# Optimization experiments

Hardware: AMD Instinct MI355X
Metric: run time of the kernel (lower is better)

The kernel has to match this reference:

```python
import jax, jax.numpy as jnp
import numpy as np

N_NODES = 100000
N_EDGES = 1600000
N_PAIRS = 500000
K_HOPS = 6


def _bn(x, g, b, eps):
    # training-mode batch norm over the node/edge (batch) axis, biased variance
    mu = jnp.mean(x, axis=0)
    var = jnp.var(x, axis=0)
    return (x - mu) * jax.lax.rsqrt(var + eps) * g + b


def _gelu(x):
    return jax.nn.gelu(x, approximate=False)  # torch GELU default (erf)


def setup_inputs() -> dict:
    key = jax.random.key(0)
    ks = jax.random.split(key, 20)
    F, EF = 128, 32

    def w(k, shape, s=0.05):
        return jax.random.normal(k, shape, dtype=jnp.float32) * s

    return {
        'X': jax.random.normal(ks[0], (N_NODES, F), jnp.float32),
        'Y': jax.random.normal(ks[1], (N_PAIRS, EF), jnp.float32),
        'edge_index': jax.random.randint(ks[2], (2, N_EDGES), 0, N_NODES, jnp.int32),
        'inds0': jax.random.randint(ks[3], (N_PAIRS,), 0, N_NODES, jnp.int32),
        'inds1': jax.random.randint(ks[4], (N_PAIRS,), 0, N_NODES, jnp.int32),
        'bn_node_g': jnp.ones((F,), jnp.float32),
        'bn_node_b': jnp.zeros((F,), jnp.float32),
        'tag_lin_W': w(ks[5], (F, 128)),
        'tag_lin_b': jnp.zeros((128,), jnp.float32),
        'tag_Ws': w(ks[6], (K_HOPS + 1, 128, 128)),
        'tag_bias': jnp.zeros((128,), jnp.float32),
        'nl_W0': w(ks[7], (256, 256)),
        'nl_b0': jnp.zeros((256,), jnp.float32),
        'nl_W1': w(ks[8], (256, 128)),
        'nl_b1': jnp.zeros((128,), jnp.float32),
        'cl_W': w(ks[9], (128, 128)),
        'cl_b': jnp.zeros((128,), jnp.float32),
        'end_W': w(ks[10], (128, 8)),
        'end_b': jnp.zeros((8,), jnp.float32),
        'bn_edge_g': jnp.ones((544,), jnp.float32),
        'bn_edge_b': jnp.zeros((544,), jnp.float32),
        'el_W0': w(ks[11], (544, 512)),
        'el_b0': jnp.zeros((512,), jnp.float32),
        'el_W1': w(ks[12], (512, 256)),
        'el_b1': jnp.zeros((256,), jnp.float32),
        'el_end_W': w(ks[13], (256, 1)),
        'el_end_b': jnp.zeros((1,), jnp.float32),
    }


def reference(X, Y, bn_node_g, bn_node_b, tag_lin_W, tag_lin_b, tag_Ws, tag_bias,
              nl_W0, nl_b0, nl_W1, nl_b1, cl_W, cl_b, end_W, end_b,
              bn_edge_g, bn_edge_b, el_W0, el_b0, el_W1, el_b1, el_end_W, el_end_b,
              edge_index, inds0, inds1):
    N = X.shape[0]
    # ---- NodeGLAM ----
    x = _bn(X, bn_node_g, bn_node_b, 1e-5)
    # TagModule: Linear -> GELU -> TAGConv -> GELU
    h = _gelu(x @ tag_lin_W + tag_lin_b)
    src, dst = edge_index[0], edge_index[1]
    # gcn_norm (no self loops): deg over target, norm = d^-1/2[src]*d^-1/2[dst]
    deg = jax.ops.segment_sum(jnp.ones(src.shape, h.dtype), dst, num_segments=N)
    dinv = jnp.where(deg > 0, jax.lax.rsqrt(jnp.maximum(deg, 1.0)), 0.0)
    wgt = (dinv[src] * dinv[dst])[:, None]  # [E,1]
    out = h @ tag_Ws[0]
    hk = h
    for k in range(1, K_HOPS + 1):
        hk = jax.ops.segment_sum(hk[src] * wgt, dst, num_segments=N)  # gather-scale-scatter
        out = out + hk @ tag_Ws[k]
    h = _gelu(out + tag_bias)
    a = jnp.concatenate([x, h], axis=1)  # [N, 256]
    a = _gelu(a @ nl_W0 + nl_b0)
    a = _gelu(a @ nl_W1 + nl_b1)  # Node_embs [N,128]
    cl = _gelu(a @ cl_W + cl_b)
    node_classes = jax.nn.softmax(cl @ end_W + end_b, axis=-1)  # [N,8]
    # ---- edge feature gather + EdgeGLAM ----
    Omega = jnp.concatenate([a[inds0], a[inds1], X[inds0], X[inds1], Y], axis=1)  # [P,544]
    o = _bn(Omega, bn_edge_g, bn_edge_b, 1.0)  # BatchNorm(input_, output_) -> eps=1
    o = _gelu(o @ el_W0 + el_b0)
    o = _gelu(o @ el_W1 + el_b1)
    e_pred = jax.nn.sigmoid(o @ el_end_W + el_end_b)[:, 0]  # [P]
    return (node_classes, e_pred)
```

## Files before the change

### kernel.cpp

```cpp
#include <hip/hip_runtime.h>
#include <math.h>

#define NN 100000
#define NE 1600000
#define NP 500000
#define KHOPS 6
#define ECHK 50000
#define NB_SCAN ((NN + 1023) / 1024)

typedef unsigned short u16;
typedef short bf16x8 __attribute__((ext_vector_type(8)));
typedef float f32x4 __attribute__((ext_vector_type(4)));

__device__ __forceinline__ float gelu_erf(float x) {
    return 0.5f * x * (1.0f + erff(x * 0.70710678118654752f));
}
__device__ __forceinline__ float b2f(u16 u) {
    return __uint_as_float(((unsigned int)u) << 16);
}
__device__ __forceinline__ u16 f2b(float f) {
    unsigned int x = __float_as_uint(f);
    return (u16)((x + 0x7FFFu + ((x >> 16) & 1u)) >> 16);
}
__device__ __forceinline__ bf16x8 cvt8(float4 a, float4 b) {
    bf16x8 v;
    v[0]=(short)f2b(a.x); v[1]=(short)f2b(a.y); v[2]=(short)f2b(a.z); v[3]=(short)f2b(a.w);
    v[4]=(short)f2b(b.x); v[5]=(short)f2b(b.y); v[6]=(short)f2b(b.z); v[7]=(short)f2b(b.w);
    return v;
}

template<int BF>
__global__ void col_stats(const void* __restrict__ Matv, int rows, int lc,
                          const int* __restrict__ w0, const int* __restrict__ w1,
                          float* __restrict__ sums, float* __restrict__ sumsq,
                          int base0, int base1)
{
    __shared__ float red[256];
    const int t = threadIdx.x;
    const int C = 1 << lc;
    const long total = (long)rows << lc;
    const long stride = (long)gridDim.x * 256;
    float s0 = 0.f, q0 = 0.f, s1 = 0.f, q1 = 0.f;
    for (long idx = (long)blockIdx.x * 256 + t; idx < total; idx += stride) {
        int r = (int)(idx >> lc);
        float v = BF ? b2f(((const u16*)Matv)[idx]) : ((const float*)Matv)[idx];
        float f0 = w0 ? (float)w0[r] : 1.0f;
        s0 += f0 * v;
        q0 += f0 * v * v;
        if (w1) {
            float f1 = (float)w1[r];
            s1 += f1 * v;
            q1 += f1 * v * v;
        }
    }
    red[t] = s0; __syncthreads();
    if (t < C) { float x = 0.f; for (int k = t; k < 256; k += C) x += red[k]; atomicAdd(&sums[base0 + t], x); }
    __syncthreads();
    red[t] = q0; __syncthreads();
    if (t < C) { float x = 0.f; for (int k = t; k < 256; k += C) x += red[k]; atomicAdd(&sumsq[base0 + t], x); }
    __syncthreads();
    if (w1) {
        red[t] = s1; __syncthreads();
        if (t < C) { float x = 0.f; for (int k = t; k < 256; k += C) x += red[k]; atomicAdd(&sums[base1 + t], x); }
        __syncthreads();
        red[t] = q1; __syncthreads();
        if (t < C) { float x = 0.f; for (int k = t; k < 256; k += C) x += red[k]; atomicAdd(&sumsq[base1 + t], x); }
    }
}

__global__ void bn_finalize(const float* __restrict__ sums, const float* __restrict__ sumsq,
                            const float* __restrict__ g, const float* __restrict__ b,
                            float* __restrict__ s, float* __restrict__ t,
                            int C, float count, float eps)
{
    int c = blockIdx.x * blockDim.x + threadIdx.x;
    if (c < C) {
        float mu = sums[c] / count;
        float var = sumsq[c] / count - mu * mu;
        float sc = g[c] * rsqrtf(var + eps);
        s[c] = sc;
        t[c] = b[c] - mu * sc;
    }
}

__global__ void hist_add(const int* __restrict__ idx, int n, int* __restrict__ cnt)
{
    int stride = gridDim.x * blockDim.x;
    for (int i = blockIdx.x * blockDim.x + threadIdx.x; i < n; i += stride)
        atomicAdd(&cnt[idx[i]], 1);
}

__global__ void hist_add2(const int* __restrict__ i0, const int* __restrict__ i1, int n,
                          int* __restrict__ c0, int* __restrict__ c1)
{
    int stride = gridDim.x * blockDim.x;
    for (int i = blockIdx.x * blockDim.x + threadIdx.x; i < n; i += stride) {
        atomicAdd(&c0[i0[i]], 1);
        atomicAdd(&c1[i1[i]], 1);
    }
}

__global__ void scan1(const int* __restrict__ cnt, int* __restrict__ ex,
                      int* __restrict__ part, int n)
{
    __shared__ int buf[1024];
    int b = blockIdx.x, t = threadIdx.x;
    int i = b * 1024 + t;
    int v = (i < n) ? cnt[i] : 0;
    buf[t] = v;
    __syncthreads();
    int incl = v;
    for (int o = 1; o < 1024; o <<= 1) {
        int tmp = (t >= o) ? buf[t - o] : 0;
        __syncthreads();
        incl += tmp;
        buf[t] = incl;
        __syncthreads();
    }
    if (i < n) ex[i] = incl - v;
    if (t == 1023) part[b] = incl;
}

__global__ void scan2(int* __restrict__ part, int nb)
{
    __shared__ int s[256];
    int t = threadIdx.x;
    if (t < nb) s[t] = part[t];
    __syncthreads();
    if (t == 0) {
        int run = 0;
        for (int b = 0; b < nb; ++b) { int x = s[b]; part[b] = run; run += x; }
        part[nb] = run;
    }
}

__global__ void scan3(int* __restrict__ indptr, const int* __restrict__ part,
                      const int* __restrict__ cnt, float* __restrict__ dinv, int n)
{
    int b = blockIdx.x, t = threadIdx.x;
    int i = b * 1024 + t;
    if (i < n) {
        indptr[i] += part[b];
        int c = cnt[i];
        dinv[i] = (c > 0) ? rsqrtf((float)c) : 0.f;
    }
    if (b == 0 && t == 0) indptr[n] = part[NB_SCAN];
}

__global__ void csr_build(const int* __restrict__ src, const int* __restrict__ dst, int n,
                          const int* __restrict__ indptr, int* __restrict__ cursor,
                          int* __restrict__ csrS)
{
    int stride = gridDim.x * blockDim.x;
    for (int e = blockIdx.x * blockDim.x + threadIdx.x; e < n; e += stride) {
        int s = src[e], d = dst[e];
        int pos = indptr[d] + atomicAdd(&cursor[d], 1);
        csrS[pos] = s;
    }
}

__global__ void spmm_hop(const u16* __restrict__ hin, u16* __restrict__ hout,
                         const int* __restrict__ indptr, const int* __restrict__ csrS,
                         const float* __restrict__ dinv)
{
    int gid = blockIdx.x * blockDim.x + threadIdx.x;
    int node = gid >> 6;
    int lane = gid & 63;
    if (node >= NN) return;
    float dn = dinv[node];
    int beg = indptr[node], end = indptr[node + 1];
    float a0 = 0.f, a1 = 0.f;
    int e = beg;
    for (; e + 7 < end; e += 8) {
        int sidx[8];
        ushort2 pv[8];
#pragma unroll
        for (int u = 0; u < 8; ++u) sidx[u] = csrS[e + u];
#pragma unroll
        for (int u = 0; u < 8; ++u)
            pv[u] = *(const ushort2*)(hin + (size_t)sidx[u] * 128 + lane * 2);
#pragma unroll
        for (int u = 0; u < 8; ++u) {
            float wv = dn * dinv[sidx[u]];
            a0 = fmaf(wv, b2f(pv[u].x), a0);
            a1 = fmaf(wv, b2f(pv[u].y), a1);
        }
    }
    for (; e < end; ++e) {
        int s0 = csrS[e];
        float w0 = dn * dinv[s0];
        ushort2 p0 = *(const ushort2*)(hin + (size_t)s0 * 128 + lane * 2);
        a0 = fmaf(w0, b2f(p0.x), a0);
        a1 = fmaf(w0, b2f(p0.y), a1);
    }
    ushort2 o;
    o.x = f2b(a0); o.y = f2b(a1);
    *(ushort2*)(hout + (size_t)node * 128 + lane * 2) = o;
}

__global__ void convTB(const float* __restrict__ in, u16* __restrict__ out,
                       int K, int Nc, int B)
{
    int per = K * Nc;
    int i = blockIdx.x * blockDim.x + threadIdx.x;
    if (i < per * B) {
        int m = i / per, r = i - m * per;
        int n = r / K, k = r - n * K;
        out[i] = f2b(in[(size_t)m * per + (size_t)k * Nc + n]);
    }
}

__global__ void conv_pair(const float* __restrict__ Ws, u16* __restrict__ out)
{
    int i = blockIdx.x * blockDim.x + threadIdx.x;
    if (i < 3 * 128 * 256) {
        int p = i >> 15;
        int r = i & 32767;
        int n = r >> 8, k = r & 255;
        int hop = 2 * p + (k >> 7);
        out[i] = f2b(Ws[(size_t)hop * 16384 + (size_t)(k & 127) * 128 + n]);
    }
}

__global__ void convB(const float* __restrict__ in, u16* __restrict__ out, int n4)
{
    int stride = gridDim.x * blockDim.x;
    for (int i = blockIdx.x * blockDim.x + threadIdx.x; i < n4; i += stride) {
        float4 v = ((const float4*)in)[i];
        ushort4 o;
        o.x = f2b(v.x); o.y = f2b(v.y); o.z = f2b(v.z); o.w = f2b(v.w);
        ((ushort4*)out)[i] = o;
    }
}

__global__ void fold_wT(const float* __restrict__ W0, const float* __restrict__ s,
                        u16* __restrict__ out)
{
    int i = blockIdx.x * blockDim.x + threadIdx.x;
    if (i < 512 * 544) {
        int n = i / 544, k = i - n * 544;
        out[i] = f2b(s[k] * W0[(size_t)k * 512 + n]);
    }
}

__global__ void fold_b(const float* __restrict__ W0, const float* __restrict__ b0,
                       const float* __restrict__ tv, float* __restrict__ bp)
{
    int j = blockIdx.x * blockDim.x + threadIdx.x;
    if (j < 512) {
        float s = b0[j];
        for (int k = 0; k < 544; ++k) s = fmaf(tv[k], W0[k * 512 + j], s);
        bp[j] = s;
    }
}

template<int AMODE>
__device__ __forceinline__ bf16x8 load_a_slot(
    const void* __restrict__ A0v, const void* __restrict__ A1v,
    const float* __restrict__ Yp, const int* __restrict__ i0s, const int* __restrict__ i1s,
    int rowOffset, const float* __restrict__ sv, const float* __restrict__ tv,
    int row, int r, int k0, int sl, int Mr, int lda)
{
    bf16x8 val = {0, 0, 0, 0, 0, 0, 0, 0};
    if (row < Mr) {
        if (AMODE == 0) {
            val = *(const bf16x8*)((const u16*)A0v + (size_t)row * lda + k0 + sl * 8);
        } else if (AMODE == 5) {
            int c = k0 + sl * 8;
            const u16* Ap = (c < 128) ? (const u16*)A0v : (const u16*)A1v;
            val = *(const bf16x8*)(Ap + (size_t)row * 128 + (c & 127));
        } else if (AMODE == 1) {
            int c = k0 + sl * 8;
            if (c < 128) {
                const float* xp = (const float*)A0v + (size_t)row * 128 + c;
                float4 x0 = *(const float4*)xp, x1 = *(const float4*)(xp + 4);
                float4 s0 = *(const float4*)(sv + c), s1 = *(const float4*)(sv + c + 4);
                float4 t0 = *(const float4*)(tv + c), t1 = *(const float4*)(tv + c + 4);
                float4 a = make_float4(fmaf(x0.x,s0.x,t0.x), fmaf(x0.y,s0.y,t0.y),
                                       fmaf(x0.z,s0.z,t0.z), fmaf(x0.w,s0.w,t0.w));
                float4 b = make_float4(fmaf(x1.x,s1.x,t1.x), fmaf(x1.y,s1.y,t1.y),
                                       fmaf(x1.z,s1.z,t1.z), fmaf(x1.w,s1.w,t1.w));
                val = cvt8(a, b);
            } else {
                val = *(const bf16x8*)((const u16*)A1v + (size_t)row * 128 + (c - 128));
            }
        } else if (AMODE == 3) {
            int c = k0 + sl * 8;
            const float* xp = (const float*)A0v + (size_t)row * 128 + c;
            float4 x0 = *(const float4*)xp, x1 = *(const float4*)(xp + 4);
            float4 s0 = *(const float4*)(sv + c), s1 = *(const float4*)(sv + c + 4);
            float4 t0 = *(const float4*)(tv + c), t1 = *(const float4*)(tv + c + 4);
            float4 a = make_float4(fmaf(x0.x,s0.x,t0.x), fmaf(x0.y,s0.y,t0.y),
                                   fmaf(x0.z,s0.z,t0.z), fmaf(x0.w,s0.w,t0.w));
            float4 b = make_float4(fmaf(x1.x,s1.x,t1.x), fmaf(x1.y,s1.y,t1.y),
                                   fmaf(x1.z,s1.z,t1.z), fmaf(x1.w,s1.w,t1.w));
            val = cvt8(a, b);
        } else {
            int seg = k0 >> 7;
            int c = (k0 & 127) + sl * 8;
            if (seg == 0) {
                val = *(const bf16x8*)((const u16*)A0v + (size_t)i0s[r] * 128 + c);
            } else if (seg == 1) {
                val = *(const bf16x8*)((const u16*)A0v + (size_t)i1s[r] * 128 + c);
            } else if (seg == 2) {
                val = *(const bf16x8*)((const u16*)A1v + (size_t)i0s[r] * 128 + c);
            } else if (seg == 3) {
                val = *(const bf16x8*)((const u16*)A1v + (size_t)i1s[r] * 128 + c);
            } else {
                const float* yp = Yp + (size_t)(rowOffset + row) * 32 + sl * 8;
                val = cvt8(*(const float4*)yp, *(const float4*)(yp + 4));
            }
        }
    }
    return val;
}

template<int AMODE, int ACT, int ACCUM, int OUTBF>
__launch_bounds__(256, 2)
__global__ void gemm_mfma(const void* __restrict__ A0v, const void* __restrict__ A1v,
                          const float* __restrict__ Yp,
                          const int* __restrict__ I0, const int* __restrict__ I1,
                          int rowOffset,
                          const float* __restrict__ sv, const float* __restrict__ tv,
                          const u16* __restrict__ Wb, const float* __restrict__ bias,
                          void* __restrict__ Cv, const float* __restrict__ Cacc,
                          int Mr, int Kd, int Nc, int lda)
{
    __shared__ __align__(16) u16 As[128 * 32];
    __shared__ __align__(16) u16 Bs[128 * 32];
    __shared__ int i0s[128], i1s[128];

    const int t = threadIdx.x;
    const int lane = t & 63;
    const int wid = t >> 6;
    const int wm = wid >> 1, wn = wid & 1;
    const int lb = lane & 15, lh = lane >> 4;
    const int row0 = blockIdx.x * 128;
    const int colb = blockIdx.y * 128;

    if (AMODE == 2) {
        if (t < 128) {
            int r = row0 + t;
            i0s[t] = (r < Mr) ? I0[rowOffset + r] : 0;
        } else {
            int r = row0 + (t - 128);
            i1s[t - 128] = (r < Mr) ? I1[rowOffset + r] : 0;
        }
    }

    f32x4 acc[4][4];
#pragma unroll
    for (int i = 0; i < 4; ++i)
#pragma unroll
        for (int j = 0; j < 4; ++j) acc[i][j] = (f32x4){0.f, 0.f, 0.f, 0.f};

    for (int k0 = 0; k0 < Kd; k0 += 32) {
        __syncthreads();
#pragma unroll
        for (int h = 0; h < 2; ++h) {
            int s = t + h * 256;
            int r = s >> 2, sl = s & 3;
            bf16x8 val = load_a_slot<AMODE>(A0v, A1v, Yp, i0s, i1s, rowOffset, sv, tv,
                                            row0 + r, r, k0, sl, Mr, lda);
            *(bf16x8*)&As[r * 32 + ((sl ^ ((r >> 1) & 3)) << 3)] = val;
        }
#pragma unroll
        for (int h = 0; h < 2; ++h) {
            int s = t + h * 256;
            int n = s >> 2, sl = s & 3;
            bf16x8 val = *(const bf16x8*)(Wb + (size_t)(colb + n) * Kd + k0 + sl * 8);
            *(bf16x8*)&Bs[n * 32 + ((sl ^ ((n >> 1) & 3)) << 3)] = val;
        }
        __syncthreads();
        bf16x8 af[4], bfr[4];
#pragma unroll
        for (int i = 0; i < 4; ++i) {
            int r = wm * 64 + i * 16 + lb;
            af[i] = *(const bf16x8*)&As[r * 32 + ((lh ^ ((r >> 1) & 3)) << 3)];
        }
#pragma unroll
        for (int j = 0; j < 4; ++j) {
            int n = wn * 64 + j * 16 + lb;
            bfr[j] = *(const bf16x8*)&Bs[n * 32 + ((lh ^ ((n >> 1) & 3)) << 3)];
        }
#pragma unroll
        for (int i = 0; i < 4; ++i)
#pragma unroll
            for (int j = 0; j < 4; ++j)
                acc[i][j] = __builtin_amdgcn_mfma_f32_16x16x32_bf16(af[i], bfr[j], acc[i][j], 0, 0, 0);
    }

#pragma unroll
    for (int i = 0; i < 4; ++i) {
#pragma unroll
        for (int j = 0; j < 4; ++j) {
            int col = colb + wn * 64 + j * 16 + lb;
#pragma unroll
            for (int r = 0; r < 4; ++r) {
                int row = row0 + wm * 64 + i * 16 + lh * 4 + r;
                if (row < Mr) {
                    size_t off = (size_t)row * Nc + col;
                    float v = acc[i][j][r];
                    if (ACCUM) v += Cacc[off];
                    if (ACT) v = gelu_erf(v + bias[col]);
                    if (OUTBF) ((u16*)Cv)[off] = f2b(v);
                    else       ((float*)Cv)[off] = v;
                }
            }
        }
    }
}

template<int AMODE, int ACT, int OUTBF>
__launch_bounds__(512, 4)
__global__ void gemm_wide(const void* __restrict__ A0v, const void* __restrict__ A1v,
                          const float* __restrict__ Yp,
                          const int* __restrict__ I0, const int* __restrict__ I1,
                          int rowOffset,
                          const float* __restrict__ sv, const float* __restrict__ tv,
                          const u16* __restrict__ Wb, const float* __restrict__ bias,
                          void* __restrict__ Cv, int Mr, int Kd, int Nc)
{
    __shared__ __align__(16) u16 As[128 * 32];
    __shared__ __align__(16) u16 Bs[256 * 32];
    __shared__ int i0s[128], i1s[128];

    const int t = threadIdx.x;
    const int lane = t & 63;
    const int wid = t >> 6;
    const int wm = wid >> 2, wn = wid & 3;
    const int lb = lane & 15, lh = lane >> 4;
    const int row0 = blockIdx.x * 128;
    const int colb = blockIdx.y * 256;

    if (AMODE == 2) {
        if (t < 128) {
            int r = row0 + t;
            i0s[t] = (r < Mr) ? I0[rowOffset + r] : 0;
        } else if (t < 256) {
            int r = row0 + (t - 128);
            i1s[t - 128] = (r < Mr) ? I1[rowOffset + r] : 0;
        }
    }

    f32x4 acc[4][4];
#pragma unroll
    for (int i = 0; i < 4; ++i)
#pragma unroll
        for (int j = 0; j < 4; ++j) acc[i][j] = (f32x4){0.f, 0.f, 0.f, 0.f};

    for (int k0 = 0; k0 < Kd; k0 += 32) {
        __syncthreads();
        {
            int r = t >> 2, sl = t & 3;
            bf16x8 val = load_a_slot<AMODE>(A0v, A1v, Yp, i0s, i1s, rowOffset, sv, tv,
                                            row0 + r, r, k0, sl, Mr, 0);
            *(bf16x8*)&As[r * 32 + ((sl ^ ((r >> 1) & 3)) << 3)] = val;
        }
#pragma unroll
        for (int h = 0; h < 2; ++h) {
            int s = t + h * 512;
            int n = s >> 2, sl = s & 3;
            bf16x8 val = *(const bf16x8*)(Wb + (size_t)(colb + n) * Kd + k0 + sl * 8);
            *(bf16x8*)&Bs[n * 32 + ((sl ^ ((n >> 1) & 3)) << 3)] = val;
        }
        __syncthreads();
        bf16x8 af[4], bfr[4];
#pragma unroll
        for (int i = 0; i < 4; ++i) {
            int r = wm * 64 + i * 16 + lb;
            af[i] = *(const bf16x8*)&As[r * 32 + ((lh ^ ((r >> 1) & 3)) << 3)];
        }
#pragma unroll
        for (int j = 0; j < 4; ++j) {
            int n = wn * 64 + j * 16 + lb;
            bfr[j] = *(const bf16x8*)&Bs[n * 32 + ((lh ^ ((n >> 1) & 3)) << 3)];
        }
#pragma unroll
        for (int i = 0; i < 4; ++i)
#pragma unroll
            for (int j = 0; j < 4; ++j)
                acc[i][j] = __builtin_amdgcn_mfma_f32_16x16x32_bf16(af[i], bfr[j], acc[i][j], 0, 0, 0);
    }

#pragma unroll
    for (int i = 0; i < 4; ++i) {
#pragma unroll
        for (int j = 0; j < 4; ++j) {
            int col = colb + wn * 64 + j * 16 + lb;
#pragma unroll
            for (int r = 0; r < 4; ++r) {
                int row = row0 + wm * 64 + i * 16 + lh * 4 + r;
                if (row < Mr) {
                    size_t off = (size_t)row * Nc + col;
                    float v = acc[i][j][r];
                    if (ACT) v = gelu_erf(v + bias[col]);
                    if (OUTBF) ((u16*)Cv)[off] = f2b(v);
                    else       ((float*)Cv)[off] = v;
                }
            }
        }
    }
}

__launch_bounds__(512, 4)
__global__ void gemm_head(const u16* __restrict__ A0, const u16* __restrict__ Wb,
                          const float* __restrict__ bias, const float* __restrict__ eW,
                          const float* __restrict__ eb,
                          float* __restrict__ outp, int outOffset, int Mr)
{
    __shared__ __align__(16) u16 As[128 * 32];
    __shared__ __align__(16) u16 Bs[256 * 32];
    __shared__ float bls[256], ews[256];
    __shared__ float sred[4][128];

    const int t = threadIdx.x;
    const int lane = t & 63;
    const int wid = t >> 6;
    const int wm = wid >> 2, wn = wid & 3;
    const int lb = lane & 15, lh = lane >> 4;
    const int row0 = blockIdx.x * 128;
    const int Kd = 512;

    if (t < 256) { bls[t] = bias[t]; ews[t] = eW[t]; }

    f32x4 acc[4][4];
#pragma unroll
    for (int i = 0; i < 4; ++i)
#pragma unroll
        for (int j = 0; j < 4; ++j) acc[i][j] = (f32x4){0.f, 0.f, 0.f, 0.f};

    for (int k0 = 0; k0 < Kd; k0 += 32) {
        __syncthreads();
        {
            int r = t >> 2, sl = t & 3;
            int row = row0 + r;
            bf16x8 val = {0,0,0,0,0,0,0,0};
            if (row < Mr) val = *(const bf16x8*)(A0 + (size_t)row * 512 + k0 + sl * 8);
            *(bf16x8*)&As[r * 32 + ((sl ^ ((r >> 1) & 3)) << 3)] = val;
        }
#pragma unroll
        for (int h = 0; h < 2; ++h) {
            int s = t + h * 512;
            int n = s >> 2, sl = s & 3;
            bf16x8 val = *(const bf16x8*)(Wb + (size_t)n * Kd + k0 + sl * 8);
            *(bf16x8*)&Bs[n * 32 + ((sl ^ ((n >> 1) & 3)) << 3)] = val;
        }
        __syncthreads();
        bf16x8 af[4], bfr[4];
#pragma unroll
        for (int i = 0; i < 4; ++i) {
            int r = wm * 64 + i * 16 + lb;
            af[i] = *(const bf16x8*)&As[r * 32 + ((lh ^ ((r >> 1) & 3)) << 3)];
        }
#pragma unroll
        for (int j = 0; j < 4; ++j) {
            int n = wn * 64 + j * 16 + lb;
            bfr[j] = *(const bf16x8*)&Bs[n * 32 + ((lh ^ ((n >> 1) & 3)) << 3)];
        }
#pragma unroll
        for (int i = 0; i < 4; ++i)
#pragma unroll
            for (int j = 0; j < 4; ++j)
                acc[i][j] = __builtin_amdgcn_mfma_f32_16x16x32_bf16(af[i], bfr[j], acc[i][j], 0, 0, 0);
    }

#pragma unroll
    for (int i = 0; i < 4; ++i) {
#pragma unroll
        for (int r = 0; r < 4; ++r) {
            float p = 0.f;
#pragma unroll
            for (int j = 0; j < 4; ++j) {
                int col = wn * 64 + j * 16 + lb;
                p += gelu_erf(acc[i][j][r] + bls[col]) * ews[col];
            }
            p += __shfl_xor(p, 1);
            p += __shfl_xor(p, 2);
            p += __shfl_xor(p, 4);
            p += __shfl_xor(p, 8);
            if (lb == 0) sred[wn][wm * 64 + i * 16 + lh * 4 + r] = p;
        }
    }
    __syncthreads();
    if (t < 128) {
        int row = row0 + t;
        if (row < Mr) {
            float s = sred[0][t] + sred[1][t] + sred[2][t] + sred[3][t] + eb[0];
            outp[outOffset + row] = 1.f / (1.f + expf(-s));
        }
    }
}

__global__ void node_head(const float* __restrict__ cl, const float* __restrict__ Wend,
                          const float* __restrict__ bend, float* __restrict__ out, int m)
{
    __shared__ float WsT[8 * 128];
    __shared__ float bs[8];
    int t = threadIdx.x;
    for (int i = t; i < 1024; i += 256) {
        int k = i >> 3, j = i & 7;
        WsT[j * 128 + k] = Wend[i];
    }
    if (t < 8) bs[t] = bend[t];
    __syncthreads();
    int gid = blockIdx.x * 256 + t;
    int wave = gid >> 6, lane = gid & 63;
    if (wave >= m) return;
    float v0 = cl[(size_t)wave * 128 + lane];
    float v1 = cl[(size_t)wave * 128 + lane + 64];
    float lg[8];
#pragma unroll
    for (int j = 0; j < 8; ++j) {
        float p = v0 * WsT[j * 128 + lane] + v1 * WsT[j * 128 + lane + 64];
#pragma unroll
        for (int o = 32; o; o >>= 1) p += __shfl_down(p, o);
        lg[j] = p;
    }
    if (lane == 0) {
        float mx = -1e30f;
#pragma unroll
        for (int j = 0; j < 8; ++j) { lg[j] += bs[j]; mx = fmaxf(mx, lg[j]); }
        float s = 0.f;
#pragma unroll
        for (int j = 0; j < 8; ++j) { lg[j] = expf(lg[j] - mx); s += lg[j]; }
        float inv = 1.f / s;
#pragma unroll
        for (int j = 0; j < 8; ++j) out[(size_t)wave * 8 + j] = lg[j] * inv;
    }
}

extern "C" void kernel_launch(void* const* d_in, const int* in_sizes, int n_in,
                              void* d_out, int out_size, void* d_ws, size_t ws_size,
                              hipStream_t stream)
{
    const float* X    = (const float*)d_in[0];
    const float* Y    = (const float*)d_in[1];
    const int*   EI   = (const int*)d_in[2];
    const int*   I0   = (const int*)d_in[3];
    const int*   I1   = (const int*)d_in[4];
    const float* bnG  = (const float*)d_in[5];
    const float* bnB  = (const float*)d_in[6];
    const float* Wlin = (const float*)d_in[7];
    const float* blin = (const float*)d_in[8];
    const float* tagWs= (const float*)d_in[9];
    const float* tagB = (const float*)d_in[10];
    const float* nlW0 = (const float*)d_in[11];
    const float* nlb0 = (const float*)d_in[12];
    const float* nlW1 = (const float*)d_in[13];
    const float* nlb1 = (const float*)d_in[14];
    const float* clW  = (const float*)d_in[15];
    const float* clb  = (const float*)d_in[16];
    const float* endW = (const float*)d_in[17];
    const float* endB = (const float*)d_in[18];
    const float* beG  = (const float*)d_in[19];
    const float* beB  = (const float*)d_in[20];
    const float* elW0 = (const float*)d_in[21];
    const float* elb0 = (const float*)d_in[22];
    const float* elW1 = (const float*)d_in[23];
    const float* elb1 = (const float*)d_in[24];
    const float* elEW = (const float*)d_in[25];
    const float* elEb = (const float*)d_in[26];

    const int N = NN, E = NE, P = NP;

    char* w = (char*)d_ws;
    size_t off = 0;
    auto alloc = [&](size_t bytes) -> void* {
        void* p = w + off;
        off += (bytes + 255) & ~(size_t)255;
        return p;
    };

    size_t zeroBytes = (size_t)(544 + 544 + 128 + 128) * 4 + (size_t)4 * N * 4;
    char* zr = (char*)alloc(zeroBytes);
    float* statS = (float*)zr;
    float* statQ = statS + 544;
    float* nodeS = statQ + 544;
    float* nodeQ = nodeS + 128;
    int* cnt    = (int*)(nodeQ + 128);
    int* cursor = cnt + N;
    int* cnt0   = cursor + N;
    int* cnt1   = cnt0 + N;

    int*   indptr = (int*)alloc((size_t)(N + 1) * 4);
    int*   part   = (int*)alloc((size_t)(NB_SCAN + 1) * 4);
    float* dinv   = (float*)alloc((size_t)N * 4);
    int*   csrS   = (int*)alloc((size_t)E * 4);
    float* sNode  = (float*)alloc(128 * 4);
    float* tNode  = (float*)alloc(128 * 4);
    float* sEdge  = (float*)alloc(544 * 4);
    float* tEdge  = (float*)alloc(544 * 4);
    float* b0p    = (float*)alloc(512 * 4);
    u16* Wlinb  = (u16*)alloc((size_t)128 * 128 * 2);
    u16* tagWsPb= (u16*)alloc((size_t)3 * 128 * 256 * 2);
    u16* tagW6b = (u16*)alloc((size_t)128 * 128 * 2);
    u16* nlW0b  = (u16*)alloc((size_t)256 * 256 * 2);
    u16* nlW1b  = (u16*)alloc((size_t)128 * 256 * 2);
    u16* clWb   = (u16*)alloc((size_t)128 * 128 * 2);
    u16* elW1b  = (u16*)alloc((size_t)256 * 512 * 2);
    u16* W0pb   = (u16*)alloc((size_t)512 * 544 * 2);
    u16*   hA   = (u16*)alloc((size_t)N * 128 * 2);
    u16*   hB   = (u16*)alloc((size_t)N * 128 * 2);
    float* outT = (float*)alloc((size_t)N * 128 * 4);

    if (ws_size < off) return;

    u16*   aEmb  = hA;
    u16*   houtb = hB;
    float* out_nodes = (float*)d_out;
    float* out_epred = (float*)d_out + (size_t)N * 8;

    hipMemsetAsync(zr, 0, zeroBytes, stream);

    convTB<<<(128*128 + 255)/256, 256, 0, stream>>>(Wlin, Wlinb, 128, 128, 1);
    conv_pair<<<(3*128*256 + 255)/256, 256, 0, stream>>>(tagWs, tagWsPb);
    convTB<<<(128*128 + 255)/256, 256, 0, stream>>>(tagWs + (size_t)KHOPS*128*128, tagW6b, 128, 128, 1);
    convTB<<<(256*256 + 255)/256, 256, 0, stream>>>(nlW0, nlW0b, 256, 256, 1);
    convTB<<<(256*128 + 255)/256, 256, 0, stream>>>(nlW1, nlW1b, 256, 128, 1);
    convTB<<<(128*128 + 255)/256, 256, 0, stream>>>(clW, clWb, 128, 128, 1);
    convTB<<<(512*256 + 255)/256, 256, 0, stream>>>(elW1, elW1b, 512, 256, 1);

    col_stats<0><<<1024, 256, 0, stream>>>(X, N, 7, nullptr, nullptr, nodeS, nodeQ, 0, 0);
    bn_finalize<<<1, 128, 0, stream>>>(nodeS, nodeQ, bnG, bnB, sNode, tNode, 128, (float)N, 1e-5f);

    dim3 g1((N + 127) / 128, 1);
    gemm_mfma<3, 1, 0, 1><<<g1, 256, 0, stream>>>(X, nullptr, nullptr, nullptr, nullptr, 0,
                                                  sNode, tNode, Wlinb, blin, hA, nullptr, N, 128, 128, 128);

    hist_add<<<2048, 256, 0, stream>>>(EI + E, E, cnt);
    hist_add2<<<1024, 256, 0, stream>>>(I0, I1, P, cnt0, cnt1);
    scan1<<<NB_SCAN, 1024, 0, stream>>>(cnt, indptr, part, N);
    scan2<<<1, 256, 0, stream>>>(part, NB_SCAN);
    scan3<<<NB_SCAN, 1024, 0, stream>>>(indptr, part, cnt, dinv, N);
    csr_build<<<2048, 256, 0, stream>>>(EI, EI + E, E, indptr, cursor, csrS);

    int spmmGrid = (N * 64 + 255) / 256;
    spmm_hop<<<spmmGrid, 256, 0, stream>>>(hA, hB, indptr, csrS, dinv);
    gemm_mfma<5, 0, 0, 0><<<g1, 256, 0, stream>>>(hA, hB, nullptr, nullptr, nullptr, 0,
                                                  nullptr, nullptr, tagWsPb, nullptr, outT, nullptr,
                                                  N, 256, 128, 0);
    spmm_hop<<<spmmGrid, 256, 0, stream>>>(hB, hA, indptr, csrS, dinv);
    spmm_hop<<<spmmGrid, 256, 0, stream>>>(hA, hB, indptr, csrS, dinv);
    gemm_mfma<5, 0, 1, 0><<<g1, 256, 0, stream>>>(hA, hB, nullptr, nullptr, nullptr, 0,
                                                  nullptr, nullptr, tagWsPb + (size_t)1*128*256,
                                                  nullptr, outT, outT, N, 256, 128, 0);
    spmm_hop<<<spmmGrid, 256, 0, stream>>>(hB, hA, indptr, csrS, dinv);
    spmm_hop<<<spmmGrid, 256, 0, stream>>>(hA, hB, indptr, csrS, dinv);
    gemm_mfma<5, 0, 1, 0><<<g1, 256, 0, stream>>>(hA, hB, nullptr, nullptr, nullptr, 0,
                                                  nullptr, nullptr, tagWsPb + (size_t)2*128*256,
                                                  nullptr, outT, outT, N, 256, 128, 0);
    spmm_hop<<<spmmGrid, 256, 0, stream>>>(hB, hA, indptr, csrS, dinv);
    gemm_mfma<0, 1, 1, 1><<<g1, 256, 0, stream>>>(hA, nullptr, nullptr, nullptr, nullptr, 0,
                                                  nullptr, nullptr, tagW6b, tagB, houtb, outT,
                                                  N, 128, 128, 128);

    u16*   a256  = (u16*)outT;
    float* clbuf = outT;
    {
        dim3 gA((N + 127) / 128, 1);
        gemm_wide<1, 1, 1><<<gA, 512, 0, stream>>>(X, houtb, nullptr, nullptr, nullptr, 0,
                                                   sNode, tNode, nlW0b, nlb0, a256, N, 256, 256);
        dim3 gB((N + 127) / 128, 1);
        gemm_mfma<0, 1, 0, 1><<<gB, 256, 0, stream>>>(a256, nullptr, nullptr, nullptr, nullptr, 0,
                                                      nullptr, nullptr, nlW1b, nlb1, aEmb, nullptr,
                                                      N, 256, 128, 256);
        gemm_mfma<0, 1, 0, 0><<<gB, 256, 0, stream>>>(aEmb, nullptr, nullptr, nullptr, nullptr, 0,
                                                      nullptr, nullptr, clWb, clb, clbuf, nullptr,
                                                      N, 128, 128, 128);
        node_head<<<(N + 3) / 4, 256, 0, stream>>>(clbuf, endW, endB, out_nodes, N);
    }

    u16* Xb = hB;
    convB<<<2048, 256, 0, stream>>>(X, Xb, N * 128 / 4);

    col_stats<1><<<1024, 256, 0, stream>>>(aEmb, N, 7, cnt0, cnt1, statS, statQ, 0, 128);
    col_stats<1><<<1024, 256, 0, stream>>>(Xb,   N, 7, cnt0, cnt1, statS, statQ, 256, 384);
    col_stats<0><<<1024, 256, 0, stream>>>(Y,    P, 5, nullptr, nullptr, statS, statQ, 512, 0);
    bn_finalize<<<3, 256, 0, stream>>>(statS, statQ, beG, beB, sEdge, tEdge, 544, (float)P, 1.0f);
    fold_wT<<<(512*544 + 255)/256, 256, 0, stream>>>(elW0, sEdge, W0pb);
    fold_b<<<2, 256, 0, stream>>>(elW0, elb0, tEdge, b0p);

    u16* o1 = (u16*)outT;
    for (int pb = 0; pb < P; pb += ECHK) {
        int m = (P - pb < ECHK) ? (P - pb) : ECHK;
        dim3 gA((m + 127) / 128, 2);
        gemm_wide<2, 1, 1><<<gA, 512, 0, stream>>>(aEmb, Xb, Y, I0, I1, pb,
                                                   nullptr, nullptr, W0pb, b0p, o1, m, 544, 512);
        dim3 gB((m + 127) / 128, 1);
        gemm_head<<<gB, 512, 0, stream>>>(o1, elW1b, elb1, elEW, elEb, out_epred, pb, m);
    }
}
```

Baseline: 2.278 ms.

## Precompute per-edge source weights for SpMM and deepen wide GEMM K-tile

A new kernel stores dinv[src] for every CSR edge once, so each SpMM hop reads contiguous per-edge weights instead of doing a dependent random gather of dinv per neighbor. The destination scale is applied once at the end instead of per edge. Separately, the wide 512-thread GEMM now stages 64-wide K slices with an 8-slot XOR swizzle and runs two MFMA sub-steps per barrier, halving K-loop iterations and syncs, with bounds checks on K. This costs an extra E-sized float buffer and more shared memory per block, which may lower occupancy.

New measurement: 2.443 ms, median of 2. 7.2% more time.

```diff
diff --git a/kernel.cpp b/kernel.cpp
--- a/kernel.cpp
+++ b/kernel.cpp
@@ -159,9 +159,17 @@
     }
 }
 
+__global__ void make_csrw(const int* __restrict__ csrS, const float* __restrict__ dinv,
+                          float* __restrict__ csrW, int n)
+{
+    int stride = gridDim.x * blockDim.x;
+    for (int i = blockIdx.x * blockDim.x + threadIdx.x; i < n; i += stride)
+        csrW[i] = dinv[csrS[i]];
+}
+
 __global__ void spmm_hop(const u16* __restrict__ hin, u16* __restrict__ hout,
                          const int* __restrict__ indptr, const int* __restrict__ csrS,
-                         const float* __restrict__ dinv)
+                         const float* __restrict__ csrW, const float* __restrict__ dinv)
 {
     int gid = blockIdx.x * blockDim.x + threadIdx.x;
     int node = gid >> 6;
@@ -173,28 +181,29 @@
     int e = beg;
     for (; e + 7 < end; e += 8) {
         int sidx[8];
+        float wv[8];
         ushort2 pv[8];
 #pragma unroll
         for (int u = 0; u < 8; ++u) sidx[u] = csrS[e + u];
+#pragma unroll
+        for (int u = 0; u < 8; ++u) wv[u] = csrW[e + u];
 #pragma unroll
         for (int u = 0; u < 8; ++u)
             pv[u] = *(const ushort2*)(hin + (size_t)sidx[u] * 128 + lane * 2);
 #pragma unroll
         for (int u = 0; u < 8; ++u) {
-            float wv = dn * dinv[sidx[u]];
-            a0 = fmaf(wv, b2f(pv[u].x), a0);
-            a1 = fmaf(wv, b2f(pv[u].y), a1);
+            a0 = fmaf(wv[u], b2f(pv[u].x), a0);
+            a1 = fmaf(wv[u], b2f(pv[u].y), a1);
         }
     }
     for (; e < end; ++e) {
-        int s0 = csrS[e];
-        float w0 = dn * dinv[s0];
-        ushort2 p0 = *(const ushort2*)(hin + (size_t)s0 * 128 + lane * 2);
+        float w0 = csrW[e];
+        ushort2 p0 = *(const ushort2*)(hin + (size_t)csrS[e] * 128 + lane * 2);
         a0 = fmaf(w0, b2f(p0.x), a0);
         a1 = fmaf(w0, b2f(p0.y), a1);
     }
     ushort2 o;
-    o.x = f2b(a0); o.y = f2b(a1);
+    o.x = f2b(a0 * dn); o.y = f2b(a1 * dn);
     *(ushort2*)(hout + (size_t)node * 128 + lane * 2) = o;
 }
 
@@ -259,18 +268,17 @@
     const void* __restrict__ A0v, const void* __restrict__ A1v,
     const float* __restrict__ Yp, const int* __restrict__ i0s, const int* __restrict__ i1s,
     int rowOffset, const float* __restrict__ sv, const float* __restrict__ tv,
-    int row, int r, int k0, int sl, int Mr, int lda)
+    int row, int r, int k, int Mr, int Kd, int lda)
 {
     bf16x8 val = {0, 0, 0, 0, 0, 0, 0, 0};
-    if (row < Mr) {
+    if (row < Mr && k < Kd) {
         if (AMODE == 0) {
-            val = *(const bf16x8*)((const u16*)A0v + (size_t)row * lda + k0 + sl * 8);
+            val = *(const bf16x8*)((const u16*)A0v + (size_t)row * lda + k);
         } else if (AMODE == 5) {
-            int c = k0 + sl * 8;
-            const u16* Ap = (c < 128) ? (const u16*)A0v : (const u16*)A1v;
-            val = *(const bf16x8*)(Ap + (size_t)row * 128 + (c & 127));
+            const u16* Ap = (k < 128) ? (const u16*)A0v : (const u16*)A1v;
+            val = *(const bf16x8*)(Ap + (size_t)row * 128 + (k & 127));
         } else if (AMODE == 1) {
-            int c = k0 + sl * 8;
+            int c = k;
             if (c < 128) {
                 const float* xp = (const float*)A0v + (size_t)row * 128 + c;
                 float4 x0 = *(const float4*)xp, x1 = *(const float4*)(xp + 4);
@@ -285,7 +293,7 @@
                 val = *(const bf16x8*)((const u16*)A1v + (size_t)row * 128 + (c - 128));
             }
         } else if (AMODE == 3) {
-            int c = k0 + sl * 8;
+            int c = k;
             const float* xp = (const float*)A0v + (size_t)row * 128 + c;
             float4 x0 = *(const float4*)xp, x1 = *(const float4*)(xp + 4);
             float4 s0 = *(const float4*)(sv + c), s1 = *(const float4*)(sv + c + 4);
@@ -296,8 +304,8 @@
                                    fmaf(x1.z,s1.z,t1.z), fmaf(x1.w,s1.w,t1.w));
             val = cvt8(a, b);
         } else {
-            int seg = k0 >> 7;
-            int c = (k0 & 127) + sl * 8;
+            int seg = k >> 7;
+            int c = k & 127;
             if (seg == 0) {
                 val = *(const bf16x8*)((const u16*)A0v + (size_t)i0s[r] * 128 + c);
             } else if (seg == 1) {
@@ -307,7 +315,7 @@
             } else if (seg == 3) {
                 val = *(const bf16x8*)((const u16*)A1v + (size_t)i1s[r] * 128 + c);
             } else {
-                const float* yp = Yp + (size_t)(rowOffset + row) * 32 + sl * 8;
+                const float* yp = Yp + (size_t)(rowOffset + row) * 32 + c;
                 val = cvt8(*(const float4*)yp, *(const float4*)(yp + 4));
             }
         }
@@ -361,7 +369,7 @@
             int s = t + h * 256;
             int r = s >> 2, sl = s & 3;
             bf16x8 val = load_a_slot<AMODE>(A0v, A1v, Yp, i0s, i1s, rowOffset, sv, tv,
-                                            row0 + r, r, k0, sl, Mr, lda);
+                                            row0 + r, r, k0 + sl * 8, Mr, Kd, lda);
             *(bf16x8*)&As[r * 32 + ((sl ^ ((r >> 1) & 3)) << 3)] = val;
         }
 #pragma unroll
@@ -421,8 +429,8 @@
                           const u16* __restrict__ Wb, const float* __restrict__ bias,
                           void* __restrict__ Cv, int Mr, int Kd, int Nc)
 {
-    __shared__ __align__(16) u16 As[128 * 32];
-    __shared__ __align__(16) u16 Bs[256 * 32];
+    __shared__ __align__(16) u16 As[128 * 64];
+    __shared__ __align__(16) u16 Bs[256 * 64];
     __shared__ int i0s[128], i1s[128];
 
     const int t = threadIdx.x;
@@ -449,38 +457,46 @@
 #pragma unroll
         for (int j = 0; j < 4; ++j) acc[i][j] = (f32x4){0.f, 0.f, 0.f, 0.f};
 
-    for (int k0 = 0; k0 < Kd; k0 += 32) {
+    for (int k0 = 0; k0 < Kd; k0 += 64) {
         __syncthreads();
-        {
-            int r = t >> 2, sl = t & 3;
-            bf16x8 val = load_a_slot<AMODE>(A0v, A1v, Yp, i0s, i1s, rowOffset, sv, tv,
-                                            row0 + r, r, k0, sl, Mr, 0);
-            *(bf16x8*)&As[r * 32 + ((sl ^ ((r >> 1) & 3)) << 3)] = val;
-        }
 #pragma unroll
         for (int h = 0; h < 2; ++h) {
             int s = t + h * 512;
-            int n = s >> 2, sl = s & 3;
-            bf16x8 val = *(const bf16x8*)(Wb + (size_t)(colb + n) * Kd + k0 + sl * 8);
-            *(bf16x8*)&Bs[n * 32 + ((sl ^ ((n >> 1) & 3)) << 3)] = val;
+            int r = s >> 3, sl = s & 7;
+            bf16x8 val = load_a_slot<AMODE>(A0v, A1v, Yp, i0s, i1s, rowOffset, sv, tv,
+                                            row0 + r, r, k0 + sl * 8, Mr, Kd, 0);
+            *(bf16x8*)&As[r * 64 + ((sl ^ ((r >> 1) & 7)) << 3)] = val;
+        }
+#pragma unroll
+        for (int h = 0; h < 4; ++h) {
+            int s = t + h * 512;
+            int n = s >> 3, sl = s & 7;
+            int k = k0 + sl * 8;
+            bf16x8 val = {0,0,0,0,0,0,0,0};
+            if (k < Kd) val = *(const bf16x8*)(Wb + (size_t)(colb + n) * Kd + k);
+            *(bf16x8*)&Bs[n * 64 + ((sl ^ ((n >> 1) & 7)) << 3)] = val;
         }
         __syncthreads();
-        bf16x8 af[4], bfr[4];
-#pragma unroll
-        for (int i = 0; i < 4; ++i) {
-            int r = wm * 64 + i * 16 + lb;
-            af[i] = *(const bf16x8*)&As[r * 32 + ((lh ^ ((r >> 1) & 3)) << 3)];
-        }
-#pragma unroll
-        for (int j = 0; j < 4; ++j) {
-            int n = wn * 64 + j * 16 + lb;
-            bfr[j] = *(const bf16x8*)&Bs[n * 32 + ((lh ^ ((n >> 1) & 3)) << 3)];
-        }
-#pragma unroll
-        for (int i = 0; i < 4; ++i)
-#pragma unroll
-            for (int j = 0; j < 4; ++j)
-                acc[i][j] = __builtin_amdgcn_mfma_f32_16x16x32_bf16(af[i], bfr[j], acc[i][j], 0, 0, 0);
+#pragma unroll
+        for (int kk = 0; kk < 64; kk += 32) {
+            int sb = kk >> 3;
+            bf16x8 af[4], bfr[4];
+#pragma unroll
+            for (int i = 0; i < 4; ++i) {
+                int r = wm * 64 + i * 16 + lb;
+                af[i] = *(const bf16x8*)&As[r * 64 + (((sb + lh) ^ ((r >> 1) & 7)) << 3)];
+            }
+#pragma unroll
+            for (int j = 0; j < 4; ++j) {
+                int n = wn * 64 + j * 16 + lb;
+                bfr[j] = *(const bf16x8*)&Bs[n * 64 + (((sb + lh) ^ ((n >> 1) & 7)) << 3)];
+            }
+#pragma unroll
+            for (int i = 0; i < 4; ++i)
+#pragma unroll
+                for (int j = 0; j < 4; ++j)
+                    acc[i][j] = __builtin_amdgcn_mfma_f32_16x16x32_bf16(af[i], bfr[j], acc[i][j], 0, 0, 0);
+        }
     }
 
 #pragma unroll
@@ -687,6 +703,7 @@
     int*   part   = (int*)alloc((size_t)(NB_SCAN + 1) * 4);
     float* dinv   = (float*)alloc((size_t)N * 4);
     int*   csrS   = (int*)alloc((size_t)E * 4);
+    float* csrW   = (float*)alloc((size_t)E * 4);
     float* sNode  = (float*)alloc(128 * 4);
     float* tNode  = (float*)alloc(128 * 4);
     float* sEdge  = (float*)alloc(544 * 4);
@@ -734,23 +751,24 @@
     scan2<<<1, 256, 0, stream>>>(part, NB_SCAN);
     scan3<<<NB_SCAN, 1024, 0, stream>>>(indptr, part, cnt, dinv, N);
     csr_build<<<2048, 256, 0, stream>>>(EI, EI + E, E, indptr, cursor, csrS);
+    make_csrw<<<2048, 256, 0, stream>>>(csrS, dinv, csrW, E);
 
     int spmmGrid = (N * 64 + 255) / 256;
-    spmm_hop<<<spmmGrid, 256, 0, stream>>>(hA, hB, indptr, csrS, dinv);
+    spmm_hop<<<spmmGrid, 256, 0, stream>>>(hA, hB, indptr, csrS, csrW, dinv);
     gemm_mfma<5, 0, 0, 0><<<g1, 256, 0, stream>>>(hA, hB, nullptr, nullptr, nullptr, 0,
                                                   nullptr, nullptr, tagWsPb, nullptr, outT, nullptr,
                                                   N, 256, 128, 0);
-    spmm_hop<<<spmmGrid, 256, 0, stream>>>(hB, hA, indptr, csrS, dinv);
-    spmm_hop<<<spmmGrid, 256, 0, stream>>>(hA, hB, indptr, csrS, dinv);
+    spmm_hop<<<spmmGrid, 256, 0, stream>>>(hB, hA, indptr, csrS, csrW, dinv);
+    spmm_hop<<<spmmGrid, 256, 0, stream>>>(hA, hB, indptr, csrS, csrW, dinv);
     gemm_mfma<5, 0, 1, 0><<<g1, 256, 0, stream>>>(hA, hB, nullptr, nullptr, nullptr, 0,
                                                   nullptr, nullptr, tagWsPb + (size_t)1*128*256,
                                                   nullptr, outT, outT, N, 256, 128, 0);
-    spmm_hop<<<spmmGrid, 256, 0, stream>>>(hB, hA, indptr, csrS, dinv);
-    spmm_hop<<<spmmGrid, 256, 0, stream>>>(hA, hB, indptr, csrS, dinv);
+    spmm_hop<<<spmmGrid, 256, 0, stream>>>(hB, hA, indptr, csrS, csrW, dinv);
+    spmm_hop<<<spmmGrid, 256, 0, stream>>>(hA, hB, indptr, csrS, csrW, dinv);
     gemm_mfma<5, 0, 1, 0><<<g1, 256, 0, stream>>>(hA, hB, nullptr, nullptr, nullptr, 0,
                                                   nullptr, nullptr, tagWsPb + (size_t)2*128*256,
                                                   nullptr, outT, outT, N, 256, 128, 0);
-    spmm_hop<<<spmmGrid, 256, 0, stream>>>(hB, hA, indptr, csrS, dinv);
+    spmm_hop<<<spmmGrid, 256, 0, stream>>>(hB, hA, indptr, csrS, csrW, dinv);
     gemm_mfma<0, 1, 1, 1><<<g1, 256, 0, stream>>>(hA, nullptr, nullptr, nullptr, nullptr, 0,
                                                   nullptr, nullptr, tagW6b, tagB, houtb, outT,
                                                   N, 128, 128, 128);
```
